# Performance work log

Measured on AMD Instinct MI355X. Metric: run time of the kernel, lower is better.

Reference implementation:

```python
import jax, jax.numpy as jnp
import numpy as np

S = 128          # hidden mul for 0e and 1o in the GVP
M_OUT = 256      # 2*n_dets*el_emb_dim = 2*8*16
N_DETS = 8
FACTOR = 2 * N_DETS  # mul_to_axis factor = 16
EPS = 1e-8


def _gvp_layer(s, v, Wh, Wu, Wm, bm, activate):
    # s: (..., S) scalars (0e); v: (..., S, 3) vectors (1o)
    Vh = jnp.einsum('...mt,mh->...ht', v, Wh)                 # hidden vectors
    vn = jnp.sqrt(jnp.sum(Vh * Vh, axis=-1) + EPS)            # invariant norms
    sm = jnp.concatenate([s, vn], axis=-1) @ Wm + bm          # scalar channel
    Vu = jnp.einsum('...ht,ho->...ot', Vh, Wu)
    if activate:
        return jax.nn.silu(sm), Vu * jax.nn.sigmoid(sm)[..., None]
    return sm, Vu  # activate_final=False


def _gvp_mlp(x, params):
    s = x[..., :S]
    v = x[..., S:].reshape(x.shape[:-1] + (S, 3))
    n = len(params)
    for i, (Wh, Wu, Wm, bm) in enumerate(params):
        s, v = _gvp_layer(s, v, Wh, Wu, Wm, bm, activate=(i < n - 1))
    return s, v


def _anti_mlp(x, params):
    # antisymmetrize_e3_func: odd part under parity (1o components negated)
    s1, v1 = _gvp_mlp(x, params)
    xp = jnp.concatenate([x[..., :S], -x[..., S:]], axis=-1)
    s2, v2 = _gvp_mlp(xp, params)
    return 0.5 * (s1 - s2), 0.5 * (v1 - v2)


def setup_inputs() -> dict:
    key = jax.random.key(0)
    ks = jax.random.split(key, 11)
    B, NEL = 2048, 16
    f32 = jnp.float32
    inp = {
        'mo_coeffs': jax.random.normal(ks[0], (B, NEL, S * 4), dtype=f32),
        # GVP layer 0
        'Wh0': jax.random.normal(ks[1], (S, S), f32) / np.sqrt(S),
        'Wu0': jax.random.normal(ks[2], (S, S), f32) / np.sqrt(S),
        'Wm0': jax.random.normal(ks[3], (2 * S, S), f32) / np.sqrt(2 * S),
        'bm0': jnp.zeros((S,), f32),
        # GVP layer 1 (final, no activation)
        'Wh1': jax.random.normal(ks[4], (S, S), f32) / np.sqrt(S),
        'Wu1': jax.random.normal(ks[5], (S, S), f32) / np.sqrt(S),
        'Wm1': jax.random.normal(ks[6], (2 * S, S), f32) / np.sqrt(2 * S),
        'bm1': jnp.zeros((S,), f32),
        # NamedE3Linear: one weight per irrep block (0e and 1o)
        'W0': jax.random.normal(ks[7], (S, M_OUT), f32),
        'W1': jax.random.normal(ks[8], (S, M_OUT), f32),
    }
    return inp


def reference(mo_coeffs, Wh0, Wu0, Wm0, bm0, Wh1, Wu1, Wm1, bm1, W0, W1):
    params = [(Wh0, Wu0, Wm0, bm0), (Wh1, Wu1, Wm1, bm1)]
    s, v = _anti_mlp(mo_coeffs, params)           # (...,128), (...,128,3)
    inv_sqrt = 1.0 / np.sqrt(S).astype(np.float32)
    so = (s @ W0) * inv_sqrt                      # (..., 256)   0e block
    vo = jnp.einsum('...mt,mn->...nt', v, W1) * inv_sqrt  # (...,256,3) 1o block
    lead = so.shape[:-1]
    # mul_to_axis(16): mul 256 -> (16, 16); per-irrep flat dims concatenated
    so = so.reshape(lead + (FACTOR, M_OUT // FACTOR))            # (...,16,16)
    vo = vo.reshape(lead + (FACTOR, (M_OUT // FACTOR) * 3))      # (...,16,48)
    bf = jnp.concatenate([so, vo], axis=-1)                      # (...,16,64)
    # final reshape: (..., 2*n_dets, d) -> (..., 2, n_dets, d)
    bf = bf.reshape(lead + (2, N_DETS, bf.shape[-1]))
    return bf
```

## Files before the change

kernel.cpp:

```cpp
#include <hip/hip_runtime.h>
#include <hip/hip_bf16.h>


typedef __attribute__((ext_vector_type(8))) short short8;
typedef __attribute__((ext_vector_type(4))) float floatx4;

static __device__ __forceinline__ unsigned short f2bf(float f) {
  unsigned u = __float_as_uint(f);
  u = (u + 0x7fffu + ((u >> 16) & 1u)) >> 16;
  return (unsigned short)u;
}
static __device__ __forceinline__ unsigned pk2(float lo, float hi) {
  __hip_bfloat162 h = __float22bfloat162_rn(make_float2(lo, hi));
  return *(unsigned*)&h;
}

static __device__ __forceinline__ void put_sw(unsigned short* B, int k, int n,
                                              float val, int KT) {
  int kt = k >> 5, quad = (k >> 3) & 3, j = k & 7;
  int nt = n >> 4, c = n & 15;
  int lane = quad * 16 + c;
  B[(((nt * KT + kt) * 64 + lane) << 3) + j] = f2bf(val);
}

__global__ __launch_bounds__(128) void prep1(
    const float* __restrict__ Wh0, const float* __restrict__ Wu0,
    const float* __restrict__ Wh1, const float* __restrict__ Wu1,
    unsigned short* __restrict__ Wcat_sw, float* __restrict__ T) {
  int b = blockIdx.x, o = threadIdx.x;
  if (b < 128) {
    int m = b;
    float acc = 0.f;
    for (int h = 0; h < 128; ++h) acc += Wh0[m * 128 + h] * Wu0[h * 128 + o];
    put_sw(Wcat_sw, m, o, Wh0[m * 128 + o], 4);
    put_sw(Wcat_sw, m, o + 128, acc, 4);
  } else {
    int m = b - 128;
    float acc = 0.f;
    for (int h = 0; h < 128; ++h) acc += Wh1[m * 128 + h] * Wu1[h * 128 + o];
    T[m * 128 + o] = acc;
  }
}

__global__ __launch_bounds__(256) void prep2(
    const float* __restrict__ T, const float* __restrict__ W1,
    const float* __restrict__ Wm0, unsigned short* __restrict__ C_sw,
    unsigned short* __restrict__ Wm0_sw) {
  int b = blockIdx.x, tid = threadIdx.x;
  if (b < 128) {
    int m = b, n = tid;
    float acc = 0.f;
    for (int h = 0; h < 128; ++h) acc += T[m * 128 + h] * W1[h * 256 + n];
    put_sw(C_sw, m, n, acc * 0.08838834764831845f, 4);
  } else {
    int k = (b - 128) * 2 + (tid >> 7);
    int n = tid & 127;
    put_sw(Wm0_sw, k, n, Wm0[k * 128 + n], 8);
  }
}

#define XA_S 264
#define XV_S 136
#define XV_T 2176

__global__ __launch_bounds__(256, 5) void main_k(
    const float* __restrict__ x, const float* __restrict__ bm0,
    const unsigned short* __restrict__ Wcat_sw,
    const unsigned short* __restrict__ Wm0_sw,
    const unsigned short* __restrict__ C_sw, float* __restrict__ out) {
  __shared__ __align__(16) unsigned char smem[21504];
  unsigned short* xv = (unsigned short*)smem;
  unsigned short* v1 = (unsigned short*)smem;
  unsigned short* xa = (unsigned short*)(smem + 13056);

  const int tid = threadIdx.x;
  const int lane = tid & 63;
  const int w = tid >> 6;
  const int l15 = lane & 15;
  const int quad = lane >> 4;
  const int r0 = blockIdx.x << 4;
  const float* xrow = x + (size_t)r0 * 512;
  float* orow = out + (size_t)r0 * 1024;
  const int ntg[4] = {2 * w, 2 * w + 1, 8 + 2 * w, 9 + 2 * w};

  float bias0 = bm0[(2 * w) * 16 + l15];
  float bias1 = bm0[(2 * w + 1) * 16 + l15];

#pragma unroll
  for (int i = 0; i < 2; ++i) {
    int e = tid + 256 * i;
    int r = e >> 5, c0 = (e & 31) << 2;
    float4 s4 = *(const float4*)(xrow + r * 512 + c0);
    uint2 p = make_uint2(pk2(s4.x, s4.y), pk2(s4.z, s4.w));
    *(uint2*)(xa + r * XA_S + c0) = p;
  }
#pragma unroll
  for (int i = 0; i < 2; ++i) {
    int e = tid + 256 * i;
    int r = e >> 5, mc = e & 31;
    const float* p = xrow + r * 512 + 128 + mc * 12;
    float4 a = *(const float4*)(p);
    float4 b = *(const float4*)(p + 4);
    float4 c = *(const float4*)(p + 8);
    float f[12] = {a.x, a.y, a.z, a.w, b.x, b.y, b.z, b.w, c.x, c.y, c.z, c.w};
#pragma unroll
    for (int t = 0; t < 3; ++t) {
      uint2 pk = make_uint2(pk2(f[t], f[t + 3]), pk2(f[t + 6], f[t + 9]));
      *(uint2*)(xv + t * XV_T + r * XV_S + mc * 4) = pk;
    }
  }
  __syncthreads();

  const floatx4 zf4 = {0.f, 0.f, 0.f, 0.f};

  floatx4 accH[3][2];
#pragma unroll
  for (int t = 0; t < 3; ++t)
#pragma unroll
    for (int j = 0; j < 2; ++j) accH[t][j] = zf4;
  for (int kt = 0; kt < 4; ++kt) {
    short8 bf[2];
#pragma unroll
    for (int j = 0; j < 2; ++j)
      bf[j] = *(const short8*)(Wcat_sw + (((ntg[j] * 4 + kt) * 64 + lane) << 3));
#pragma unroll
    for (int t = 0; t < 3; ++t) {
      short8 af = *(const short8*)(xv + t * XV_T + l15 * XV_S + kt * 32 + quad * 8);
#pragma unroll
      for (int j = 0; j < 2; ++j)
        accH[t][j] = __builtin_amdgcn_mfma_f32_16x16x32_bf16(af, bf[j], accH[t][j], 0, 0, 0);
    }
  }

#pragma unroll
  for (int j = 0; j < 2; ++j)
#pragma unroll
    for (int rg = 0; rg < 4; ++rg) {
      float s0 = accH[0][j][rg], s1 = accH[1][j][rg], s2 = accH[2][j][rg];
      float vn = sqrtf(s0 * s0 + s1 * s1 + s2 * s2 + 1e-8f);
      int r = quad * 4 + rg;
      int h = ntg[j] * 16 + l15;
      xa[r * XA_S + 128 + h] = f2bf(vn);
    }

  floatx4 accU[3][2];
#pragma unroll
  for (int t = 0; t < 3; ++t)
#pragma unroll
    for (int j = 0; j < 2; ++j) accU[t][j] = zf4;
  for (int kt = 0; kt < 4; ++kt) {
    short8 bf[2];
#pragma unroll
    for (int j = 0; j < 2; ++j)
      bf[j] = *(const short8*)(Wcat_sw + (((ntg[2 + j] * 4 + kt) * 64 + lane) << 3));
#pragma unroll
    for (int t = 0; t < 3; ++t) {
      short8 af = *(const short8*)(xv + t * XV_T + l15 * XV_S + kt * 32 + quad * 8);
#pragma unroll
      for (int j = 0; j < 2; ++j)
        accU[t][j] = __builtin_amdgcn_mfma_f32_16x16x32_bf16(af, bf[j], accU[t][j], 0, 0, 0);
    }
  }
  __syncthreads();

  floatx4 ga[2] = {zf4, zf4};
  for (int kt = 0; kt < 8; ++kt) {
    short8 af = *(const short8*)(xa + l15 * XA_S + kt * 32 + quad * 8);
    short8 b0 = *(const short8*)(Wm0_sw + ((((2 * w) * 8 + kt) * 64 + lane) << 3));
    short8 b1 = *(const short8*)(Wm0_sw + ((((2 * w + 1) * 8 + kt) * 64 + lane) << 3));
    ga[0] = __builtin_amdgcn_mfma_f32_16x16x32_bf16(af, b0, ga[0], 0, 0, 0);
    ga[1] = __builtin_amdgcn_mfma_f32_16x16x32_bf16(af, b1, ga[1], 0, 0, 0);
  }
  float g[2][4];
#pragma unroll
  for (int j = 0; j < 2; ++j) {
    float bias = j ? bias1 : bias0;
#pragma unroll
    for (int rg = 0; rg < 4; ++rg)
      g[j][rg] = 1.f / (1.f + __expf(-(ga[j][rg] + bias)));
  }
#pragma unroll
  for (int t = 0; t < 3; ++t)
#pragma unroll
    for (int j = 0; j < 2; ++j)
#pragma unroll
      for (int rg = 0; rg < 4; ++rg) {
        int r = quad * 4 + rg;
        int o = (2 * w + j) * 16 + l15;
        v1[t * XV_T + r * XV_S + o] = f2bf(accU[t][j][rg] * g[j][rg]);
      }
  __syncthreads();

#pragma unroll
  for (int i = 0; i < 4; ++i) {
    int e = tid + 256 * i;
    int r = e >> 6, gblk = (e >> 2) & 15, s4i = e & 3;
    *(floatx4*)(orow + (size_t)r * 1024 + gblk * 64 + s4i * 4) = zf4;
  }

#pragma unroll
  for (int half = 0; half < 2; ++half) {
    floatx4 vacc[3][2];
#pragma unroll
    for (int t = 0; t < 3; ++t)
#pragma unroll
      for (int j = 0; j < 2; ++j) vacc[t][j] = zf4;
    for (int kt = 0; kt < 4; ++kt) {
      short8 bf[2];
#pragma unroll
      for (int j = 0; j < 2; ++j)
        bf[j] = *(const short8*)(C_sw +
                                 (((ntg[2 * half + j] * 4 + kt) * 64 + lane) << 3));
#pragma unroll
      for (int t = 0; t < 3; ++t) {
        short8 af = *(const short8*)(v1 + t * XV_T + l15 * XV_S + kt * 32 + quad * 8);
#pragma unroll
        for (int j = 0; j < 2; ++j)
          vacc[t][j] = __builtin_amdgcn_mfma_f32_16x16x32_bf16(af, bf[j], vacc[t][j], 0, 0, 0);
      }
    }
#pragma unroll
    for (int j = 0; j < 2; ++j) {
      int nt = ntg[2 * half + j];
#pragma unroll
      for (int rg = 0; rg < 4; ++rg) {
        int r = quad * 4 + rg;
        *(float3*)(orow + (size_t)r * 1024 + nt * 64 + 16 + 3 * l15) =
            make_float3(vacc[0][j][rg], vacc[1][j][rg], vacc[2][j][rg]);
      }
    }
  }
}

extern "C" void kernel_launch(void* const* d_in, const int* in_sizes, int n_in,
                              void* d_out, int out_size, void* d_ws,
                              size_t ws_size, hipStream_t stream) {
  const float* mo = (const float*)d_in[0];
  const float* Wh0 = (const float*)d_in[1];
  const float* Wu0 = (const float*)d_in[2];
  const float* Wm0 = (const float*)d_in[3];
  const float* bm0 = (const float*)d_in[4];
  const float* Wh1 = (const float*)d_in[5];
  const float* Wu1 = (const float*)d_in[6];
  const float* W1 = (const float*)d_in[10];

  unsigned short* ws = (unsigned short*)d_ws;
  unsigned short* Wcat_sw = ws;
  unsigned short* C_sw = ws + 32768;
  unsigned short* Wm0_sw = ws + 65536;
  float* T = (float*)(ws + 98304);

  prep1<<<256, 128, 0, stream>>>(Wh0, Wu0, Wh1, Wu1, Wcat_sw, T);
  prep2<<<256, 256, 0, stream>>>(T, W1, Wm0, C_sw, Wm0_sw);

  main_k<<<2048, 256, 0, stream>>>(mo, bm0, Wcat_sw, Wm0_sw, C_sw,
                                   (float*)d_out);
}
```

Before: 231.7 us.

## Process two row tiles per block with register-staged prefetch of the next input

Each block now handles two 16-row tiles instead of one, halving the grid. The second tile's global loads are issued into registers before the first tile's compute, then written to separate LDS buffers while the back half of the first tile runs. The aim is to hide global load latency behind MFMA work. Barriers are replaced with raw lgkmcnt waits plus s_barrier. In exchange, LDS per block grows, the occupancy hint drops from 5 to 4 blocks, and staging takes more registers.

Measured after the change: 262.1 us. 13.1% more time.

```diff
diff --git a/kernel.cpp b/kernel.cpp
--- a/kernel.cpp
+++ b/kernel.cpp
@@ -63,45 +63,49 @@
 #define XV_S 136
 #define XV_T 2176
 
-__global__ __launch_bounds__(256, 5) void main_k(
-    const float* __restrict__ x, const float* __restrict__ bm0,
-    const unsigned short* __restrict__ Wcat_sw,
-    const unsigned short* __restrict__ Wm0_sw,
-    const unsigned short* __restrict__ C_sw, float* __restrict__ out) {
-  __shared__ __align__(16) unsigned char smem[21504];
-  unsigned short* xv = (unsigned short*)smem;
-  unsigned short* v1 = (unsigned short*)smem;
-  unsigned short* xa = (unsigned short*)(smem + 13056);
-
-  const int tid = threadIdx.x;
-  const int lane = tid & 63;
-  const int w = tid >> 6;
-  const int l15 = lane & 15;
-  const int quad = lane >> 4;
-  const int r0 = blockIdx.x << 4;
-  const float* xrow = x + (size_t)r0 * 512;
-  float* orow = out + (size_t)r0 * 1024;
-  const int ntg[4] = {2 * w, 2 * w + 1, 8 + 2 * w, 9 + 2 * w};
-
-  float bias0 = bm0[(2 * w) * 16 + l15];
-  float bias1 = bm0[(2 * w + 1) * 16 + l15];
-
+static __device__ __forceinline__ void lds_barrier() {
+  __builtin_amdgcn_sched_barrier(0);
+  asm volatile("s_waitcnt lgkmcnt(0)" ::: "memory");
+  __builtin_amdgcn_s_barrier();
+  __builtin_amdgcn_sched_barrier(0);
+}
+
+static __device__ __forceinline__ void load_x(const float* __restrict__ xrow,
+                                              int tid, float4* st_s,
+                                              float4* st_v) {
 #pragma unroll
   for (int i = 0; i < 2; ++i) {
     int e = tid + 256 * i;
     int r = e >> 5, c0 = (e & 31) << 2;
-    float4 s4 = *(const float4*)(xrow + r * 512 + c0);
-    uint2 p = make_uint2(pk2(s4.x, s4.y), pk2(s4.z, s4.w));
-    *(uint2*)(xa + r * XA_S + c0) = p;
+    st_s[i] = *(const float4*)(xrow + r * 512 + c0);
   }
 #pragma unroll
   for (int i = 0; i < 2; ++i) {
     int e = tid + 256 * i;
     int r = e >> 5, mc = e & 31;
     const float* p = xrow + r * 512 + 128 + mc * 12;
-    float4 a = *(const float4*)(p);
-    float4 b = *(const float4*)(p + 4);
-    float4 c = *(const float4*)(p + 8);
+    st_v[3 * i + 0] = *(const float4*)(p);
+    st_v[3 * i + 1] = *(const float4*)(p + 4);
+    st_v[3 * i + 2] = *(const float4*)(p + 8);
+  }
+}
+
+static __device__ __forceinline__ void stage_write(int tid, const float4* st_s,
+                                                   const float4* st_v,
+                                                   unsigned short* xa,
+                                                   unsigned short* xv) {
+#pragma unroll
+  for (int i = 0; i < 2; ++i) {
+    int e = tid + 256 * i;
+    int r = e >> 5, c0 = (e & 31) << 2;
+    uint2 p = make_uint2(pk2(st_s[i].x, st_s[i].y), pk2(st_s[i].z, st_s[i].w));
+    *(uint2*)(xa + r * XA_S + c0) = p;
+  }
+#pragma unroll
+  for (int i = 0; i < 2; ++i) {
+    int e = tid + 256 * i;
+    int r = e >> 5, mc = e & 31;
+    float4 a = st_v[3 * i + 0], b = st_v[3 * i + 1], c = st_v[3 * i + 2];
     float f[12] = {a.x, a.y, a.z, a.w, b.x, b.y, b.z, b.w, c.x, c.y, c.z, c.w};
 #pragma unroll
     for (int t = 0; t < 3; ++t) {
@@ -109,8 +113,14 @@
       *(uint2*)(xv + t * XV_T + r * XV_S + mc * 4) = pk;
     }
   }
-  __syncthreads();
-
+}
+
+static __device__ __forceinline__ void compute_front(
+    const unsigned short* __restrict__ Wcat_sw,
+    const unsigned short* __restrict__ Wm0_sw, unsigned short* xa,
+    unsigned short* xv, unsigned short* v1, int lane, int w, int l15, int quad,
+    float bias0, float bias1) {
+  const int ntg[4] = {2 * w, 2 * w + 1, 8 + 2 * w, 9 + 2 * w};
   const floatx4 zf4 = {0.f, 0.f, 0.f, 0.f};
 
   floatx4 accH[3][2];
@@ -161,7 +171,7 @@
         accU[t][j] = __builtin_amdgcn_mfma_f32_16x16x32_bf16(af, bf[j], accU[t][j], 0, 0, 0);
     }
   }
-  __syncthreads();
+  lds_barrier();
 
   floatx4 ga[2] = {zf4, zf4};
   for (int kt = 0; kt < 8; ++kt) {
@@ -189,15 +199,19 @@
         int o = (2 * w + j) * 16 + l15;
         v1[t * XV_T + r * XV_S + o] = f2bf(accU[t][j][rg] * g[j][rg]);
       }
-  __syncthreads();
-
+}
+
+static __device__ __forceinline__ void compute_back(
+    const unsigned short* __restrict__ C_sw, const unsigned short* v1,
+    float* __restrict__ orow, int tid, int lane, int w, int l15, int quad) {
+  const int ntg[4] = {2 * w, 2 * w + 1, 8 + 2 * w, 9 + 2 * w};
+  const floatx4 zf4 = {0.f, 0.f, 0.f, 0.f};
 #pragma unroll
   for (int i = 0; i < 4; ++i) {
     int e = tid + 256 * i;
     int r = e >> 6, gblk = (e >> 2) & 15, s4i = e & 3;
     *(floatx4*)(orow + (size_t)r * 1024 + gblk * 64 + s4i * 4) = zf4;
   }
-
 #pragma unroll
   for (int half = 0; half < 2; ++half) {
     floatx4 vacc[3][2];
@@ -230,6 +244,52 @@
       }
     }
   }
+}
+
+__global__ __launch_bounds__(256, 4) void main_k(
+    const float* __restrict__ x, const float* __restrict__ bm0,
+    const unsigned short* __restrict__ Wcat_sw,
+    const unsigned short* __restrict__ Wm0_sw,
+    const unsigned short* __restrict__ C_sw, float* __restrict__ out) {
+  __shared__ __align__(16) unsigned char smem[34560];
+  unsigned short* v1 = (unsigned short*)smem;
+  unsigned short* xa = (unsigned short*)(smem + 13056);
+  unsigned short* xv = (unsigned short*)(smem + 21504);
+
+  const int tid = threadIdx.x;
+  const int lane = tid & 63;
+  const int w = tid >> 6;
+  const int l15 = lane & 15;
+  const int quad = lane >> 4;
+  const int g0 = blockIdx.x;
+  const int g1 = blockIdx.x + 1024;
+  const float* xrow0 = x + (size_t)g0 * 16 * 512;
+  const float* xrow1 = x + (size_t)g1 * 16 * 512;
+  float* orow0 = out + (size_t)g0 * 16 * 1024;
+  float* orow1 = out + (size_t)g1 * 16 * 1024;
+
+  float bias0 = bm0[(2 * w) * 16 + l15];
+  float bias1 = bm0[(2 * w + 1) * 16 + l15];
+
+  float4 st_s[2], st_v[6];
+
+  load_x(xrow0, tid, st_s, st_v);
+  stage_write(tid, st_s, st_v, xa, xv);
+  lds_barrier();
+
+  load_x(xrow1, tid, st_s, st_v);
+
+  compute_front(Wcat_sw, Wm0_sw, xa, xv, v1, lane, w, l15, quad, bias0, bias1);
+  lds_barrier();
+
+  stage_write(tid, st_s, st_v, xa, xv);
+
+  compute_back(C_sw, v1, orow0, tid, lane, w, l15, quad);
+  lds_barrier();
+
+  compute_front(Wcat_sw, Wm0_sw, xa, xv, v1, lane, w, l15, quad, bias0, bias1);
+  lds_barrier();
+  compute_back(C_sw, v1, orow1, tid, lane, w, l15, quad);
 }
 
 extern "C" void kernel_launch(void* const* d_in, const int* in_sizes, int n_in,
@@ -253,6 +313,6 @@
   prep1<<<256, 128, 0, stream>>>(Wh0, Wu0, Wh1, Wu1, Wcat_sw, T);
   prep2<<<256, 256, 0, stream>>>(T, W1, Wm0, C_sw, Wm0_sw);
 
-  main_k<<<2048, 256, 0, stream>>>(mo, bm0, Wcat_sw, Wm0_sw, C_sw,
+  main_k<<<1024, 256, 0, stream>>>(mo, bm0, Wcat_sw, Wm0_sw, C_sw,
                                    (float*)d_out);
 }
```
